# Kernel optimization log

Measured on AMD Instinct MI355X. Metric: run time of the kernel, lower is better.

Reference implementation:

```python
import jax, jax.numpy as jnp
import numpy as np

N_EMBD = 1024
N_EXPERTS = 8
TOP_K = 2
D_FF = 4 * N_EMBD


def setup_inputs() -> dict:
    key = jax.random.key(0)
    ks = jax.random.split(key, 6)
    B, S = 4, 2048
    s = 1.0 / np.sqrt(N_EMBD)
    sf = 1.0 / np.sqrt(D_FF)
    x = jax.random.normal(ks[0], (B, S, N_EMBD), dtype=jnp.float32)
    router_w = jax.random.uniform(ks[1], (N_EMBD, N_EXPERTS), minval=-s, maxval=s, dtype=jnp.float32)
    wfc = jax.random.uniform(ks[2], (N_EXPERTS, N_EMBD, D_FF), minval=-s, maxval=s, dtype=jnp.float32)
    bfc = jax.random.uniform(ks[3], (N_EXPERTS, D_FF), minval=-s, maxval=s, dtype=jnp.float32)
    wproj = jax.random.uniform(ks[4], (N_EXPERTS, D_FF, N_EMBD), minval=-sf, maxval=sf, dtype=jnp.float32)
    bproj = jax.random.uniform(ks[5], (N_EXPERTS, N_EMBD), minval=-sf, maxval=sf, dtype=jnp.float32)
    return {"x": x, "router_w": router_w, "wfc": wfc, "bfc": bfc, "wproj": wproj, "bproj": bproj}


def reference(x, router_w, wfc, bfc, wproj, bproj):
    B, S, D = x.shape
    E = wfc.shape[0]
    xf = x.reshape(-1, D)  # [N, D] tokens
    logits = xf @ router_w  # [N, E]
    probs = jax.nn.softmax(logits.astype(jnp.float32), axis=-1)
    w, sel = jax.lax.top_k(probs, TOP_K)  # [N, K]
    w = w / jnp.sum(w, axis=-1, keepdims=True)  # norm_topk_prob
    w = w.astype(x.dtype)
    out = jnp.zeros_like(xf)
    for e in range(E):
        # per-token gate for expert e (0 if not routed here) -- same math as
        # gather -> MLP -> weighted scatter-add in the original
        gate = jnp.sum(jnp.where(sel == e, w, jnp.zeros_like(w)), axis=-1)  # [N]
        h = jax.nn.gelu(xf @ wfc[e] + bfc[e], approximate=False)  # [N, 4D]
        y = h @ wproj[e] + bproj[e]  # [N, D]
        out = out + gate[:, None] * y
    return out.reshape(B, S, D)
```

## Files before the change

kernel.cpp:

```cpp
#include <hip/hip_runtime.h>
#include <hip/hip_bf16.h>


#define N_TOK 8192
#define DMODEL 1024
#define NEXP 8
#define DFF 4096
#define CAP 8192

typedef __attribute__((ext_vector_type(8))) short short8;
typedef __attribute__((ext_vector_type(4))) float f32x4;

#define GLOAD_LDS16(g, l)                                              \
  __builtin_amdgcn_global_load_lds(                                    \
      (const __attribute__((address_space(1))) unsigned int*)(g),      \
      (__attribute__((address_space(3))) unsigned int*)(l), 16, 0, 0)

__device__ __forceinline__ unsigned short f2bf(float f) {
  unsigned u = __float_as_uint(f);
  return (unsigned short)((u + 0x7FFFu + ((u >> 16) & 1u)) >> 16);
}

__device__ __forceinline__ float gelu_f(float v) {
  return 0.5f * v * (1.0f + erff(v * 0.70710678118654752f));
}

__device__ __forceinline__ short8 pack8(float f0, float f1, float f2, float f3,
                                        float f4, float f5, float f6, float f7) {
  short8 r;
  r[0] = (short)f2bf(f0); r[1] = (short)f2bf(f1);
  r[2] = (short)f2bf(f2); r[3] = (short)f2bf(f3);
  r[4] = (short)f2bf(f4); r[5] = (short)f2bf(f5);
  r[6] = (short)f2bf(f6); r[7] = (short)f2bf(f7);
  return r;
}

__global__ void router_k(const float* __restrict__ x, const float* __restrict__ rw,
                         int* __restrict__ cnt, int* __restrict__ tok,
                         float* __restrict__ gate, unsigned short* __restrict__ xb) {
  int lane = threadIdx.x & 63;
  int t = blockIdx.x * 4 + (threadIdx.x >> 6);
  const float* xr = x + (size_t)t * DMODEL;
  unsigned short* xbr = xb + (size_t)t * DMODEL;
  float p[8];
#pragma unroll
  for (int e = 0; e < 8; ++e) p[e] = 0.0f;
#pragma unroll
  for (int j = 0; j < DMODEL / 64; ++j) {
    int i = lane + j * 64;
    float xv = xr[i];
    xbr[i] = f2bf(xv);
    const float4* r = (const float4*)(rw + (size_t)i * 8);
    float4 a = r[0], b = r[1];
    p[0] += xv * a.x; p[1] += xv * a.y; p[2] += xv * a.z; p[3] += xv * a.w;
    p[4] += xv * b.x; p[5] += xv * b.y; p[6] += xv * b.z; p[7] += xv * b.w;
  }
#pragma unroll
  for (int e = 0; e < 8; ++e) {
#pragma unroll
    for (int off = 32; off; off >>= 1) p[e] += __shfl_xor(p[e], off, 64);
  }
  if (lane == 0) {
    int e1 = 0;
#pragma unroll
    for (int e = 1; e < 8; ++e) if (p[e] > p[e1]) e1 = e;
    int e2 = (e1 == 0) ? 1 : 0;
#pragma unroll
    for (int e = 0; e < 8; ++e) if (e != e1 && p[e] > p[e2]) e2 = e;
    float w1 = 1.0f / (1.0f + expf(p[e2] - p[e1]));
    float w2 = 1.0f - w1;
    int s1 = atomicAdd(&cnt[e1], 1);
    tok[e1 * CAP + s1] = t; gate[e1 * CAP + s1] = w1;
    int s2 = atomicAdd(&cnt[e2], 1);
    tok[e2 * CAP + s2] = t; gate[e2 * CAP + s2] = w2;
  }
}

__global__ void prefix_k(const int* __restrict__ cnt, int* __restrict__ off) {
  if (threadIdx.x == 0 && blockIdx.x == 0) {
    int s = 0;
    for (int e = 0; e < NEXP; ++e) { off[e] = s; s += cnt[e]; }
  }
}

__global__ __launch_bounds__(256) void cvt_wt_k(const float* __restrict__ W,
                                                unsigned short* __restrict__ WT,
                                                int K, int N) {
  __shared__ float ls[64][68];
  int b = blockIdx.x;
  int nkt = K >> 6, nnt = N >> 6;
  int kt = b % nkt;
  int nt = (b / nkt) % nnt;
  int e = b / (nkt * nnt);
  const float* Wb = W + (size_t)e * K * N + (size_t)(kt * 64) * N + nt * 64;
  int t = threadIdx.x;
  int nn = (t & 15) * 4, kr = t >> 4;
#pragma unroll
  for (int i = 0; i < 4; ++i) {
    float4 v = *(const float4*)(Wb + (size_t)(kr + 16 * i) * N + nn);
    *(float4*)&ls[kr + 16 * i][nn] = v;
  }
  __syncthreads();
  int on = t >> 2, kc = (t & 3) * 16;
  unsigned short* dst = WT + (size_t)e * N * K + (size_t)(nt * 64 + on) * K + kt * 64 + kc;
  short8 r0, r1;
#pragma unroll
  for (int j = 0; j < 8; ++j) r0[j] = (short)f2bf(ls[kc + j][on]);
#pragma unroll
  for (int j = 0; j < 8; ++j) r1[j] = (short)f2bf(ls[kc + 8 + j][on]);
  *(short8*)dst = r0;
  *(short8*)(dst + 8) = r1;
}

#define STAGE(buf, kk)                                              \
  do {                                                              \
    GLOAD_LDS16(gA0 + (kk), &As[buf][(w * 32 + lr) * 32 + lc]);     \
    GLOAD_LDS16(gA1 + (kk), &As[buf][(w * 32 + 16 + lr) * 32 + lc]);\
    GLOAD_LDS16(gB0 + (kk), &Bs[buf][(w * 32 + lr) * 32 + lc]);     \
    GLOAD_LDS16(gB1 + (kk), &Bs[buf][(w * 32 + 16 + lr) * 32 + lc]);\
  } while (0)

#define COMPUTE(buf)                                                            \
  do {                                                                          \
    short8 af[4], bfv[4];                                                       \
    _Pragma("unroll") for (int i = 0; i < 4; ++i)                               \
        af[i] = *(const short8*)&As[buf][(wr * 64 + i * 16 + fr) * 32 + g * 8]; \
    _Pragma("unroll") for (int i = 0; i < 4; ++i)                               \
        bfv[i] = *(const short8*)&Bs[buf][(wc * 64 + i * 16 + fr) * 32 + g * 8];\
    _Pragma("unroll") for (int mi = 0; mi < 4; ++mi)                            \
        _Pragma("unroll") for (int ni = 0; ni < 4; ++ni)                        \
            acc[mi][ni] = __builtin_amdgcn_mfma_f32_16x16x32_bf16(              \
                af[mi], bfv[ni], acc[mi][ni], 0, 0, 0);                         \
  } while (0)

#define SYNC()                                          \
  do {                                                  \
    asm volatile("s_waitcnt vmcnt(0)" ::: "memory");    \
    __syncthreads();                                    \
  } while (0)

__global__ __launch_bounds__(256, 4) void gemm1a_k(
    const unsigned short* __restrict__ xb, const unsigned short* __restrict__ wT,
    const float* __restrict__ bfc, const int* __restrict__ cnt,
    const int* __restrict__ off, const int* __restrict__ tok,
    unsigned short* __restrict__ h) {
  int bid = (int)(blockIdx.x & 7) * ((int)gridDim.x >> 3) + (int)(blockIdx.x >> 3);
  int mt = bid & 63;
  int nt = (bid >> 6) & 31;
  int e = bid >> 11;
  int Me = cnt[e];
  if (mt * 128 >= Me) return;
  int base = off[e];
  int n0 = nt * 128;

  __shared__ __align__(16) unsigned short As[2][128 * 32];
  __shared__ __align__(16) unsigned short Bs[2][128 * 32];

  int tid = threadIdx.x;
  int lane = tid & 63, w = tid >> 6;
  int lr = lane >> 2;
  int lc = (lane & 3) * 8;

  int ar0i = mt * 128 + w * 32 + lr;
  int ar1i = ar0i + 16;
  int t0 = tok[e * CAP + ((ar0i < Me) ? ar0i : (Me - 1))];
  int t1 = tok[e * CAP + ((ar1i < Me) ? ar1i : (Me - 1))];
  const unsigned short* gA0 = xb + (size_t)t0 * DMODEL + lc;
  const unsigned short* gA1 = xb + (size_t)t1 * DMODEL + lc;
  const unsigned short* gB0 = wT + ((size_t)e * DFF + n0 + w * 32 + lr) * DMODEL + lc;
  const unsigned short* gB1 = gB0 + (size_t)16 * DMODEL;

  int wr = w >> 1, wc = w & 1;
  int g = lane >> 4, fr = lane & 15;

  f32x4 acc[4][4];
#pragma unroll
  for (int i = 0; i < 4; ++i)
#pragma unroll
    for (int j = 0; j < 4; ++j) acc[i][j] = (f32x4)0.0f;

  STAGE(0, 0);
  SYNC();
#pragma unroll 1
  for (int k0 = 0; k0 < DMODEL; k0 += 64) {
    STAGE(1, k0 + 32);
    COMPUTE(0);
    SYNC();
    if (k0 + 64 < DMODEL) STAGE(0, k0 + 64);
    COMPUTE(1);
    SYNC();
  }

#pragma unroll
  for (int mi = 0; mi < 4; ++mi) {
    int rl = wr * 64 + mi * 16 + g * 4;
#pragma unroll
    for (int i = 0; i < 4; ++i) {
      int r = mt * 128 + rl + i;
      if (r < Me) {
        unsigned short* hrow = h + (size_t)(base + r) * DFF;
#pragma unroll
        for (int ni = 0; ni < 4; ++ni) {
          int col = n0 + wc * 64 + ni * 16 + fr;
          float v = acc[mi][ni][i] + bfc[e * DFF + col];
          hrow[col] = f2bf(gelu_f(v));
        }
      }
    }
  }
}

__global__ __launch_bounds__(256, 4) void gemm2a_k(
    const unsigned short* __restrict__ h, const unsigned short* __restrict__ wT,
    const float* __restrict__ bproj, const int* __restrict__ cnt,
    const int* __restrict__ off, const int* __restrict__ tok,
    const float* __restrict__ gate, float* __restrict__ out) {
  int bid = (int)(blockIdx.x & 7) * ((int)gridDim.x >> 3) + (int)(blockIdx.x >> 3);
  int mt = bid & 63;
  int nt = (bid >> 6) & 7;
  int e = bid >> 9;
  int Me = cnt[e];
  if (mt * 128 >= Me) return;
  int base = off[e];
  int n0 = nt * 128;

  __shared__ __align__(16) unsigned short As[2][128 * 32];
  __shared__ __align__(16) unsigned short Bs[2][128 * 32];

  int tid = threadIdx.x;
  int lane = tid & 63, w = tid >> 6;
  int lr = lane >> 2;
  int lc = (lane & 3) * 8;

  const unsigned short* gA0 = h + (size_t)(base + mt * 128 + w * 32 + lr) * DFF + lc;
  const unsigned short* gA1 = gA0 + (size_t)16 * DFF;
  const unsigned short* gB0 = wT + ((size_t)e * DMODEL + n0 + w * 32 + lr) * DFF + lc;
  const unsigned short* gB1 = gB0 + (size_t)16 * DFF;

  int wr = w >> 1, wc = w & 1;
  int g = lane >> 4, fr = lane & 15;

  f32x4 acc[4][4];
#pragma unroll
  for (int i = 0; i < 4; ++i)
#pragma unroll
    for (int j = 0; j < 4; ++j) acc[i][j] = (f32x4)0.0f;

  STAGE(0, 0);
  SYNC();
#pragma unroll 1
  for (int k0 = 0; k0 < DFF; k0 += 64) {
    STAGE(1, k0 + 32);
    COMPUTE(0);
    SYNC();
    if (k0 + 64 < DFF) STAGE(0, k0 + 64);
    COMPUTE(1);
    SYNC();
  }

#pragma unroll
  for (int mi = 0; mi < 4; ++mi) {
    int rl = wr * 64 + mi * 16 + g * 4;
#pragma unroll
    for (int i = 0; i < 4; ++i) {
      int r = mt * 128 + rl + i;
      if (r < Me) {
        int tkn = tok[e * CAP + r];
        float gv = gate[e * CAP + r];
        float* orow = out + (size_t)tkn * DMODEL;
#pragma unroll
        for (int ni = 0; ni < 4; ++ni) {
          int col = n0 + wc * 64 + ni * 16 + fr;
          float v = acc[mi][ni][i] + bproj[e * DMODEL + col];
          atomicAdd(orow + col, gv * v);
        }
      }
    }
  }
}

extern "C" void kernel_launch(void* const* d_in, const int* in_sizes, int n_in,
                              void* d_out, int out_size, void* d_ws, size_t ws_size,
                              hipStream_t stream) {
  const float* x = (const float*)d_in[0];
  const float* rw = (const float*)d_in[1];
  const float* wfc = (const float*)d_in[2];
  const float* bfc = (const float*)d_in[3];
  const float* wproj = (const float*)d_in[4];
  const float* bproj = (const float*)d_in[5];
  float* out = (float*)d_out;

  char* ws = (char*)d_ws;
  int* cnt = (int*)ws;
  int* off_ = (int*)(ws + 64);
  int* tok = (int*)(ws + 4096);
  float* gate = (float*)(ws + 4096 + (size_t)NEXP * CAP * 4);
  size_t HOFF = 4096 + 2 * (size_t)NEXP * CAP * 4;
  unsigned short* h = (unsigned short*)(ws + HOFF);
  size_t HSZ = (size_t)(16384 + 128) * DFF * 2;
  size_t XOFF = HOFF + HSZ;
  size_t WOFF = XOFF + (size_t)N_TOK * DMODEL * 2;
  unsigned short* xb = (unsigned short*)(ws + XOFF);
  unsigned short* wT = (unsigned short*)(ws + WOFF);

  hipMemsetAsync(cnt, 0, 128, stream);
  hipMemsetAsync(out, 0, (size_t)out_size * 4, stream);
  router_k<<<N_TOK / 4, 256, 0, stream>>>(x, rw, cnt, tok, gate, xb);
  prefix_k<<<1, 64, 0, stream>>>(cnt, off_);
  cvt_wt_k<<<NEXP * (DMODEL / 64) * (DFF / 64), 256, 0, stream>>>(wfc, wT, DMODEL, DFF);
  gemm1a_k<<<NEXP * 32 * 64, 256, 0, stream>>>(xb, wT, bfc, cnt, off_, tok, h);
  cvt_wt_k<<<NEXP * (DFF / 64) * (DMODEL / 64), 256, 0, stream>>>(wproj, wT, DFF, DMODEL);
  gemm2a_k<<<NEXP * 8 * 64, 256, 0, stream>>>(h, wT, bproj, cnt, off_, tok, gate, out);
}
```

Before: 834.3 us.

## Pipeline GEMM K-loop with partial vmcnt waits to keep one stage in flight

Replaces the double-buffered K-loop, which drained all outstanding global loads before every barrier, with a loop that issues two stages up front and waits only until the older stage has landed (vmcnt(4)). The next stage's global-to-LDS loads therefore stay in flight while the current buffer is computed, which is meant to hide memory latency in both expert GEMMs. It adds an extra barrier per iteration and relies on the exact count of four loads per stage being right. The unused pack8 helper is also removed.

```diff
diff --git a/kernel.cpp b/kernel.cpp
--- a/kernel.cpp
+++ b/kernel.cpp
@@ -23,16 +23,6 @@
 
 __device__ __forceinline__ float gelu_f(float v) {
   return 0.5f * v * (1.0f + erff(v * 0.70710678118654752f));
-}
-
-__device__ __forceinline__ short8 pack8(float f0, float f1, float f2, float f3,
-                                        float f4, float f5, float f6, float f7) {
-  short8 r;
-  r[0] = (short)f2bf(f0); r[1] = (short)f2bf(f1);
-  r[2] = (short)f2bf(f2); r[3] = (short)f2bf(f3);
-  r[4] = (short)f2bf(f4); r[5] = (short)f2bf(f5);
-  r[6] = (short)f2bf(f6); r[7] = (short)f2bf(f7);
-  return r;
 }
 
 __global__ void router_k(const float* __restrict__ x, const float* __restrict__ rw,
@@ -133,11 +123,29 @@
                 af[mi], bfv[ni], acc[mi][ni], 0, 0, 0);                         \
   } while (0)
 
-#define SYNC()                                          \
-  do {                                                  \
-    asm volatile("s_waitcnt vmcnt(0)" ::: "memory");    \
-    __syncthreads();                                    \
-  } while (0)
+#define WAITV(n) asm volatile("s_waitcnt vmcnt(" #n ")" ::: "memory")
+#define BAR() __builtin_amdgcn_s_barrier()
+
+#define KLOOP(KTOT)                                                 \
+  STAGE(0, 0);                                                      \
+  STAGE(1, 32);                                                     \
+  {                                                                 \
+    int cur = 0;                                                    \
+    _Pragma("unroll 1") for (int k0 = 0; k0 < (KTOT)-64; k0 += 32) {\
+      WAITV(4);                                                     \
+      BAR();                                                        \
+      COMPUTE(cur);                                                 \
+      BAR();                                                        \
+      STAGE(cur, k0 + 64);                                          \
+      cur ^= 1;                                                     \
+    }                                                               \
+    WAITV(4);                                                       \
+    BAR();                                                          \
+    COMPUTE(cur);                                                   \
+    WAITV(0);                                                       \
+    BAR();                                                          \
+    COMPUTE(cur ^ 1);                                               \
+  }
 
 __global__ __launch_bounds__(256, 4) void gemm1a_k(
     const unsigned short* __restrict__ xb, const unsigned short* __restrict__ wT,
@@ -179,17 +187,7 @@
 #pragma unroll
     for (int j = 0; j < 4; ++j) acc[i][j] = (f32x4)0.0f;
 
-  STAGE(0, 0);
-  SYNC();
-#pragma unroll 1
-  for (int k0 = 0; k0 < DMODEL; k0 += 64) {
-    STAGE(1, k0 + 32);
-    COMPUTE(0);
-    SYNC();
-    if (k0 + 64 < DMODEL) STAGE(0, k0 + 64);
-    COMPUTE(1);
-    SYNC();
-  }
+  KLOOP(DMODEL);
 
 #pragma unroll
   for (int mi = 0; mi < 4; ++mi) {
@@ -246,17 +244,7 @@
 #pragma unroll
     for (int j = 0; j < 4; ++j) acc[i][j] = (f32x4)0.0f;
 
-  STAGE(0, 0);
-  SYNC();
-#pragma unroll 1
-  for (int k0 = 0; k0 < DFF; k0 += 64) {
-    STAGE(1, k0 + 32);
-    COMPUTE(0);
-    SYNC();
-    if (k0 + 64 < DFF) STAGE(0, k0 + 64);
-    COMPUTE(1);
-    SYNC();
-  }
+  KLOOP(DFF);
 
 #pragma unroll
   for (int mi = 0; mi < 4; ++mi) {
```

After: 797.4 us. 4.4% less time.
